# Optimization experiments

Hardware: AMD Instinct MI355X
Metric: run time of the kernel (lower is better)

The kernel has to match this reference:

```python
import jax, jax.numpy as jnp
import numpy as np
import math

B, S, DM, H, DH = 2, 2048, 1024, 16, 64  # batch, seq, d_model, heads, head_dim


def setup_inputs() -> dict:
    key = jax.random.key(0)
    ks = jax.random.split(key, 4)
    scale = 0.02
    return {
        "hidden_states": jax.random.normal(ks[0], (B, S, DM), jnp.float32),
        "Wq": jax.random.normal(ks[1], (DM, DM), jnp.float32) * scale,
        "bq": jnp.zeros((DM,), jnp.float32),
        "Wk": jax.random.normal(ks[2], (DM, DM), jnp.float32) * scale,
        "bk": jnp.zeros((DM,), jnp.float32),
        "Wv": jax.random.normal(ks[3], (DM, DM), jnp.float32) * scale,
        "bv": jnp.zeros((DM,), jnp.float32),
    }


def reference(hidden_states, Wq, bq, Wk, bk, Wv, bv):
    b, s, _ = hidden_states.shape

    def proj(W, bias):
        # torch Linear: x @ W.T + b, then transpose_for_scores -> [B,H,S,Dh]
        x = hidden_states @ W.T + bias
        return x.reshape(b, s, H, DH).transpose(0, 2, 1, 3)

    query = proj(Wq, bq)
    key = proj(Wk, bk)
    value = proj(Wv, bv)

    # qk_matmul input calibration stats (abs-max over whole tensor)
    q_max = jax.lax.stop_gradient(jnp.max(jnp.abs(query)))
    kT_max = jax.lax.stop_gradient(jnp.max(jnp.abs(key)))  # transpose doesn't change abs-max

    attn_weights = jnp.einsum('bhqd,bhkd->bhqk', query, key)  # [B,H,S,S]
    qk_out_max = jax.lax.stop_gradient(jnp.max(jnp.abs(attn_weights)))

    attn_weights = attn_weights / math.sqrt(DH)
    attn_weights = jax.nn.softmax(attn_weights.astype(jnp.float32), axis=-1).astype(query.dtype)
    # eval mode: dropout p=0.0; head_mask is None

    # v_matmul input stats; note source also records attn_weights abs-max as 'v_matmul_out' (faithful)
    aw_max = jax.lax.stop_gradient(jnp.max(jnp.abs(attn_weights)))
    v_max = jax.lax.stop_gradient(jnp.max(jnp.abs(value)))
    v_out_max = aw_max  # source bug: re-reads attn_weights for v_matmul_out

    attn_output = jnp.einsum('bhqk,bhkd->bhqd', attn_weights, value)
    attn_output = attn_output.transpose(0, 2, 1, 3).reshape(b, s, H * DH)
    return attn_output, q_max, kT_max, qk_out_max, aw_max, v_max, v_out_max
```

## Files before the change

### kernel.cpp

```cpp
#include <hip/hip_runtime.h>
#include <hip/hip_bf16.h>
#include <stdint.h>

typedef __attribute__((ext_vector_type(8))) short short8;
typedef __attribute__((ext_vector_type(4))) short short4v;
typedef __attribute__((ext_vector_type(4))) float f32x4;

#define MFMA(a, b, c) __builtin_amdgcn_mfma_f32_16x16x32_bf16((a), (b), (c), 0, 0, 0)

#define C1 0.18033688011112042f
#define INV_C1 5.545177444479562f

static __device__ __forceinline__ unsigned int f2bf2(float x, float y) {
  union { __hip_bfloat162 h; unsigned int u; } c;
  c.h = __float22bfloat162_rn(make_float2(x, y));
  return c.u;
}

static __device__ __forceinline__ void atomic_max_f32(float* addr, float v) {
  atomicMax((int*)addr, __float_as_int(v));
}

static __device__ __forceinline__ void gl_lds16(const void* g, void* l) {
  __builtin_amdgcn_global_load_lds(
      (const __attribute__((address_space(1))) void*)g,
      (__attribute__((address_space(3))) void*)l, 16, 0, 0);
}

__global__ __launch_bounds__(256) void k_cvt(
    const float* __restrict__ X, const float* __restrict__ Wq,
    const float* __restrict__ Wk, const float* __restrict__ Wv,
    short* __restrict__ Xb, short* __restrict__ Wb) {
  const int y = blockIdx.y;
  const float* src;
  short* dst;
  int n;
  if (y == 0) {
    src = X; dst = Xb; n = 4096 * 1024;
  } else {
    src = (y == 1) ? Wq : (y == 2) ? Wk : Wv;
    dst = Wb + (y - 1) * 1048576;
    n = 1048576;
  }
  const int i = (blockIdx.x * 256 + threadIdx.x) * 8;
  if (i >= n) return;
  const float4 a = *(const float4*)(src + i);
  const float4 b = *(const float4*)(src + i + 4);
  union { unsigned int u[4]; short8 s; } P;
  P.u[0] = f2bf2(a.x, a.y);
  P.u[1] = f2bf2(a.z, a.w);
  P.u[2] = f2bf2(b.x, b.y);
  P.u[3] = f2bf2(b.z, b.w);
  *(short8*)(dst + i) = P.s;
}

__global__ __launch_bounds__(256) void k_qkv(
    const short* __restrict__ Xb, const short* __restrict__ Wball,
    const float* __restrict__ bq, const float* __restrict__ bk,
    const float* __restrict__ bv,
    short* __restrict__ Qo, short* __restrict__ Ko, short* __restrict__ Vo,
    float* __restrict__ stats) {
  const int fid = (blockIdx.z * 32 + blockIdx.y) * 8 + blockIdx.x;
  const int sid = (fid & 7) * 96 + (fid >> 3);
  const int colb = sid & 7;
  const int zy = sid >> 3;
  const int z = zy >> 5;
  const int yb = zy & 31;

  const short* W = Wball + z * 1048576;
  const float* bias = (z == 0) ? bq : (z == 1) ? bk : bv;
  short* out = (z == 0) ? Qo : (z == 1) ? Ko : Vo;
  const bool qk = (z < 2);

  __shared__ __align__(16) short AB[8192];
  __shared__ float red[4];

  const int t = threadIdx.x;
  const int lane = t & 63;
  const int w = t >> 6;
  const int l16 = lane & 15, quad = lane >> 4;
  const int wr = (w >> 1) * 64, wc = (w & 1) * 64;
  const int row0 = yb * 128;
  const int col0 = colb * 128;

  const int grow = w * 16 + (lane >> 2);
  const int gcol = (lane & 3) * 8;
  const short* ag = Xb + (size_t)(row0 + grow) * 1024 + gcol;
  const short* bg = W + (size_t)(col0 + grow) * 1024 + gcol;
  short* al = AB + w * 512;
  short* bl = AB + 4096 + w * 512;

  const int f0o = qk ? (4096 + wc * 32) : (wr * 32);
  const int f1o = qk ? (wr * 32) : (4096 + wc * 32);

  f32x4 acc[4][4];
#pragma unroll
  for (int i = 0; i < 4; ++i)
#pragma unroll
    for (int j = 0; j < 4; ++j) acc[i][j] = {0.f, 0.f, 0.f, 0.f};

  for (int kk = 0; kk < 32; ++kk) {
    __syncthreads();
    const int k0 = kk * 32;
#pragma unroll
    for (int c = 0; c < 2; ++c) {
      gl_lds16(ag + c * 65536 + k0, al + c * 2048);
      gl_lds16(bg + c * 65536 + k0, bl + c * 2048);
    }
    __syncthreads();
    short8 fr0[4], fr1[4];
#pragma unroll
    for (int a = 0; a < 4; ++a)
      fr0[a] = *(const short8*)&AB[f0o + (a * 16 + l16) * 32 + quad * 8];
#pragma unroll
    for (int b = 0; b < 4; ++b)
      fr1[b] = *(const short8*)&AB[f1o + (b * 16 + l16) * 32 + quad * 8];
#pragma unroll
    for (int a = 0; a < 4; ++a)
#pragma unroll
      for (int b = 0; b < 4; ++b) acc[a][b] = MFMA(fr0[a], fr1[b], acc[a][b]);
  }

  const float qs = (z == 0) ? C1 : 1.0f;
  float amax = 0.f;
  if (qk) {
#pragma unroll
    for (int a = 0; a < 4; ++a) {
      const int dg = col0 + wc + a * 16 + quad * 4;
      const float4 b4 = *(const float4*)&bias[dg];
      const int h = dg >> 6, dl = dg & 63;
#pragma unroll
      for (int b = 0; b < 4; ++b) {
        const int sg = row0 + wr + b * 16 + l16;
        const float y0 = acc[a][b][0] + b4.x;
        const float y1 = acc[a][b][1] + b4.y;
        const float y2 = acc[a][b][2] + b4.z;
        const float y3 = acc[a][b][3] + b4.w;
        amax = fmaxf(amax, fmaxf(fmaxf(fabsf(y0), fabsf(y1)), fmaxf(fabsf(y2), fabsf(y3))));
        union { unsigned int u[2]; short4v s; } pk;
        pk.u[0] = f2bf2(y0 * qs, y1 * qs);
        pk.u[1] = f2bf2(y2 * qs, y3 * qs);
        const int bidx = sg >> 11, sl = sg & 2047;
        *(short4v*)&out[(size_t)(((bidx << 4) | h) * 2048 + sl) * 64 + dl] = pk.s;
      }
    }
  } else {
#pragma unroll
    for (int a = 0; a < 4; ++a) {
      const int sg = row0 + wr + a * 16 + quad * 4;
      const int bidx = sg >> 11, sl = sg & 2047;
#pragma unroll
      for (int b = 0; b < 4; ++b) {
        const int dg = col0 + wc + b * 16 + l16;
        const float bvf = bias[dg];
        const int h = dg >> 6, dl = dg & 63;
        const float y0 = acc[a][b][0] + bvf;
        const float y1 = acc[a][b][1] + bvf;
        const float y2 = acc[a][b][2] + bvf;
        const float y3 = acc[a][b][3] + bvf;
        amax = fmaxf(amax, fmaxf(fmaxf(fabsf(y0), fabsf(y1)), fmaxf(fabsf(y2), fabsf(y3))));
        union { unsigned int u[2]; short4v s; } pk;
        pk.u[0] = f2bf2(y0, y1);
        pk.u[1] = f2bf2(y2, y3);
        *(short4v*)&out[(size_t)(((bidx << 4) | h) * 64 + dl) * 2048 + sl] = pk.s;
      }
    }
  }
#pragma unroll
  for (int off = 32; off > 0; off >>= 1)
    amax = fmaxf(amax, __shfl_xor(amax, off, 64));
  if (lane == 0) red[w] = amax;
  __syncthreads();
  if (t == 0) {
    float m = fmaxf(fmaxf(red[0], red[1]), fmaxf(red[2], red[3]));
    atomic_max_f32(&stats[z], m);
  }
}

__global__ __launch_bounds__(512) void k_attn(
    const short* __restrict__ Q, const short* __restrict__ K,
    const short* __restrict__ V, float* __restrict__ O,
    float* __restrict__ stats) {
  const int fid = blockIdx.y * 16 + blockIdx.x;
  const int sid = ((fid & 7) << 6) + (fid >> 3);
  const int bh = sid >> 4;
  const int q0 = (sid & 15) << 7;
  const short* Qh = Q + (size_t)bh * 2048 * 64;
  const short* Kh = K + (size_t)bh * 2048 * 64;
  const short* Vh = V + (size_t)bh * 2048 * 64;

  __shared__ __align__(16) short Ks[64 * 72];
  __shared__ __align__(16) short Vts[64 * 72];
  __shared__ __align__(16) short Ps[8][16 * 72];
  __shared__ float redA[8], redB[8];

  const int t = threadIdx.x, lane = t & 63, w = t >> 6;
  const int l16 = lane & 15, quad = lane >> 4;
  const int srow = t >> 3, scol = (t & 7) * 8;
  short* myPs = &Ps[w][0];

  short8 bq0, bq1;
  {
    const short* qsrc = Qh + (q0 + w * 16 + l16) * 64 + quad * 8;
    bq0 = *(const short8*)qsrc;
    bq1 = *(const short8*)(qsrc + 32);
  }

  float m_lane = -1e30f, l_lane = 0.f, xmin_lane = 1e30f;
  f32x4 o_acc[4];
#pragma unroll
  for (int jn = 0; jn < 4; ++jn) o_acc[jn] = {0.f, 0.f, 0.f, 0.f};
  const f32x4 zero = {0.f, 0.f, 0.f, 0.f};

  short8 pk0 = *(const short8*)(Kh + srow * 64 + scol);
  short8 pv0 = *(const short8*)(Vh + srow * 2048 + scol);

  for (int kt = 0; kt < 32; ++kt) {
    __syncthreads();
    *(short8*)&Ks[srow * 72 + scol] = pk0;
    *(short8*)&Vts[srow * 72 + scol] = pv0;
    {
      const int ktn = (kt < 31) ? kt + 1 : 31;
      pk0 = *(const short8*)(Kh + (ktn * 64 + srow) * 64 + scol);
      pv0 = *(const short8*)(Vh + srow * 2048 + ktn * 64 + scol);
    }
    __syncthreads();

    f32x4 sacc[4];
#pragma unroll
    for (int j = 0; j < 4; ++j) {
      short8 kf0 = *(const short8*)&Ks[(j * 16 + l16) * 72 + quad * 8];
      short8 kf1 = *(const short8*)&Ks[(j * 16 + l16) * 72 + 32 + quad * 8];
      sacc[j] = MFMA(kf1, bq1, MFMA(kf0, bq0, zero));
    }

    {
      float pmax = m_lane, psum = l_lane, xmn = xmin_lane;
#pragma unroll
      for (int j = 0; j < 4; ++j) {
        const float x0 = sacc[j][0], x1 = sacc[j][1];
        const float x2 = sacc[j][2], x3 = sacc[j][3];
        pmax = fmaxf(pmax, fmaxf(fmaxf(x0, x1), fmaxf(x2, x3)));
        xmn = fminf(xmn, fminf(fminf(x0, x1), fminf(x2, x3)));
        const float e0 = exp2f(x0), e1 = exp2f(x1);
        const float e2 = exp2f(x2), e3 = exp2f(x3);
        psum += (e0 + e1) + (e2 + e3);
        union { unsigned int u[2]; short4v s; } pk;
        pk.u[0] = f2bf2(e0, e1);
        pk.u[1] = f2bf2(e2, e3);
        *(short4v*)&myPs[l16 * 72 + j * 16 + quad * 4] = pk.s;
      }
      m_lane = pmax;
      l_lane = psum;
      xmin_lane = xmn;
    }
    asm volatile("" ::: "memory");

#pragma unroll
    for (int tstep = 0; tstep < 2; ++tstep) {
      short8 ap = *(const short8*)&myPs[l16 * 72 + tstep * 32 + quad * 8];
#pragma unroll
      for (int jn = 0; jn < 4; ++jn) {
        short8 vf = *(const short8*)&Vts[(jn * 16 + l16) * 72 + tstep * 32 + quad * 8];
        o_acc[jn] = MFMA(ap, vf, o_acc[jn]);
      }
    }
    asm volatile("" ::: "memory");
  }

  float l = l_lane;
  l += __shfl_xor(l, 16, 64);
  l += __shfl_xor(l, 32, 64);
  float m = m_lane;
  m = fmaxf(m, __shfl_xor(m, 16, 64));
  m = fmaxf(m, __shfl_xor(m, 32, 64));
  float xm = xmin_lane;
  xm = fminf(xm, __shfl_xor(xm, 16, 64));
  xm = fminf(xm, __shfl_xor(xm, 32, 64));
  float aw = exp2f(m) / l;
  float qkx = fmaxf(m, -xm);

  const int bidx = bh >> 4, h = bh & 15;
  float linv[4];
#pragma unroll
  for (int r = 0; r < 4; ++r)
    linv[r] = 1.0f / __shfl(l, quad * 4 + r, 16);
#pragma unroll
  for (int jn = 0; jn < 4; ++jn) {
    const int d = jn * 16 + l16;
#pragma unroll
    for (int r = 0; r < 4; ++r) {
      const int s_row = q0 + w * 16 + quad * 4 + r;
      O[((size_t)(bidx * 2048 + s_row) * 1024) + h * 64 + d] =
          o_acc[jn][r] * linv[r];
    }
  }

#pragma unroll
  for (int off = 32; off > 0; off >>= 1) {
    qkx = fmaxf(qkx, __shfl_xor(qkx, off, 64));
    aw = fmaxf(aw, __shfl_xor(aw, off, 64));
  }
  if (lane == 0) {
    redA[w] = qkx;
    redB[w] = aw;
  }
  __syncthreads();
  if (t == 0) {
    float a = redA[0], b = redB[0];
#pragma unroll
    for (int i = 1; i < 8; ++i) {
      a = fmaxf(a, redA[i]);
      b = fmaxf(b, redB[i]);
    }
    atomic_max_f32(&stats[3], a * INV_C1);
    atomic_max_f32(&stats[4], b);
  }
}

__global__ void k_fin(const float* __restrict__ stats, float* __restrict__ out) {
  const int i = threadIdx.x;
  if (i == 0) out[0] = stats[0];
  if (i == 1) out[1] = stats[1];
  if (i == 2) out[2] = stats[3];
  if (i == 3) out[3] = stats[4];
  if (i == 4) out[4] = stats[2];
  if (i == 5) out[5] = stats[4];
}

extern "C" void kernel_launch(void* const* d_in, const int* in_sizes, int n_in,
                              void* d_out, int out_size, void* d_ws, size_t ws_size,
                              hipStream_t stream) {
  const float* X = (const float*)d_in[0];
  const float* Wq = (const float*)d_in[1];
  const float* bq = (const float*)d_in[2];
  const float* Wk = (const float*)d_in[3];
  const float* bk = (const float*)d_in[4];
  const float* Wv = (const float*)d_in[5];
  const float* bv = (const float*)d_in[6];
  float* out = (float*)d_out;

  float* stats = (float*)d_ws;
  short* base = (short*)((char*)d_ws + 4096);
  short* Qb = base;
  short* Kb = base + 4194304;
  short* Vb = base + 8388608;
  short* Xb = base + 12582912;
  short* Wb = base + 16777216;

  k_cvt<<<dim3(2048, 4), 256, 0, stream>>>(X, Wq, Wk, Wv, Xb, Wb);
  k_qkv<<<dim3(8, 32, 3), 256, 0, stream>>>(Xb, Wb, bq, bk, bv, Qb, Kb, Vb, stats);
  k_attn<<<dim3(16, 32), 512, 0, stream>>>(Qb, Kb, Vb, out, stats);
  k_fin<<<1, 64, 0, stream>>>(stats, out + 4194304);
}
```

Before: 208.7 us.

## Shrink attention blocks to 4 waves and load K fragments directly into registers

The attention kernel now runs 256-thread blocks, each covering 64 query rows, so twice as many blocks are launched and occupancy is hinted at 4 blocks per CU. The K tile is no longer staged in shared memory. Each lane loads its MFMA K fragments straight from global memory into registers and prefetches the next tile's fragments after the QK MFMAs. This removes LDS traffic for K and shrinks shared memory, at the cost of more register pressure and every wave loading K separately from global/L2 instead of sharing it.

```diff
diff --git a/kernel.cpp b/kernel.cpp
--- a/kernel.cpp
+++ b/kernel.cpp
@@ -177,26 +177,25 @@
   }
 }
 
-__global__ __launch_bounds__(512) void k_attn(
+__global__ __launch_bounds__(256, 4) void k_attn(
     const short* __restrict__ Q, const short* __restrict__ K,
     const short* __restrict__ V, float* __restrict__ O,
     float* __restrict__ stats) {
-  const int fid = blockIdx.y * 16 + blockIdx.x;
-  const int sid = ((fid & 7) << 6) + (fid >> 3);
-  const int bh = sid >> 4;
-  const int q0 = (sid & 15) << 7;
+  const int fid = blockIdx.y * 32 + blockIdx.x;
+  const int sid = ((fid & 7) << 7) + (fid >> 3);
+  const int bh = sid >> 5;
+  const int q0 = (sid & 31) << 6;
   const short* Qh = Q + (size_t)bh * 2048 * 64;
   const short* Kh = K + (size_t)bh * 2048 * 64;
   const short* Vh = V + (size_t)bh * 2048 * 64;
 
-  __shared__ __align__(16) short Ks[64 * 72];
   __shared__ __align__(16) short Vts[64 * 72];
-  __shared__ __align__(16) short Ps[8][16 * 72];
-  __shared__ float redA[8], redB[8];
+  __shared__ __align__(16) short Ps[4][16 * 72];
+  __shared__ float redA[4], redB[4];
 
   const int t = threadIdx.x, lane = t & 63, w = t >> 6;
   const int l16 = lane & 15, quad = lane >> 4;
-  const int srow = t >> 3, scol = (t & 7) * 8;
+  const int srow = t >> 2, scol = (t & 3) * 16;
   short* myPs = &Ps[w][0];
 
   short8 bq0, bq1;
@@ -206,32 +205,47 @@
     bq1 = *(const short8*)(qsrc + 32);
   }
 
+  const short* kg = Kh + l16 * 64 + quad * 8;
+
   float m_lane = -1e30f, l_lane = 0.f, xmin_lane = 1e30f;
   f32x4 o_acc[4];
 #pragma unroll
   for (int jn = 0; jn < 4; ++jn) o_acc[jn] = {0.f, 0.f, 0.f, 0.f};
   const f32x4 zero = {0.f, 0.f, 0.f, 0.f};
 
-  short8 pk0 = *(const short8*)(Kh + srow * 64 + scol);
   short8 pv0 = *(const short8*)(Vh + srow * 2048 + scol);
+  short8 pv1 = *(const short8*)(Vh + srow * 2048 + scol + 8);
+  short8 kf[4][2];
+#pragma unroll
+  for (int j = 0; j < 4; ++j)
+#pragma unroll
+    for (int hk = 0; hk < 2; ++hk)
+      kf[j][hk] = *(const short8*)(kg + j * 1024 + hk * 32);
 
   for (int kt = 0; kt < 32; ++kt) {
     __syncthreads();
-    *(short8*)&Ks[srow * 72 + scol] = pk0;
     *(short8*)&Vts[srow * 72 + scol] = pv0;
+    *(short8*)&Vts[srow * 72 + scol + 8] = pv1;
+    const int ktn = (kt < 31) ? kt + 1 : 31;
     {
-      const int ktn = (kt < 31) ? kt + 1 : 31;
-      pk0 = *(const short8*)(Kh + (ktn * 64 + srow) * 64 + scol);
-      pv0 = *(const short8*)(Vh + srow * 2048 + ktn * 64 + scol);
+      const short* vsrc = Vh + srow * 2048 + ktn * 64 + scol;
+      pv0 = *(const short8*)vsrc;
+      pv1 = *(const short8*)(vsrc + 8);
     }
     __syncthreads();
 
     f32x4 sacc[4];
 #pragma unroll
-    for (int j = 0; j < 4; ++j) {
-      short8 kf0 = *(const short8*)&Ks[(j * 16 + l16) * 72 + quad * 8];
-      short8 kf1 = *(const short8*)&Ks[(j * 16 + l16) * 72 + 32 + quad * 8];
-      sacc[j] = MFMA(kf1, bq1, MFMA(kf0, bq0, zero));
+    for (int j = 0; j < 4; ++j)
+      sacc[j] = MFMA(kf[j][1], bq1, MFMA(kf[j][0], bq0, zero));
+
+    {
+      const short* kgn = kg + ktn * 4096;
+#pragma unroll
+      for (int j = 0; j < 4; ++j)
+#pragma unroll
+        for (int hk = 0; hk < 2; ++hk)
+          kf[j][hk] = *(const short8*)(kgn + j * 1024 + hk * 32);
     }
 
     {
@@ -240,8 +254,8 @@
       for (int j = 0; j < 4; ++j) {
         const float x0 = sacc[j][0], x1 = sacc[j][1];
         const float x2 = sacc[j][2], x3 = sacc[j][3];
-        pmax = fmaxf(pmax, fmaxf(fmaxf(x0, x1), fmaxf(x2, x3)));
-        xmn = fminf(xmn, fminf(fminf(x0, x1), fminf(x2, x3)));
+        pmax = fmaxf(fmaxf(x0, fmaxf(x1, x2)), fmaxf(x3, pmax));
+        xmn = fminf(fminf(x0, fminf(x1, x2)), fminf(x3, xmn));
         const float e0 = exp2f(x0), e1 = exp2f(x1);
         const float e2 = exp2f(x2), e3 = exp2f(x3);
         psum += (e0 + e1) + (e2 + e3);
@@ -307,12 +321,8 @@
   }
   __syncthreads();
   if (t == 0) {
-    float a = redA[0], b = redB[0];
-#pragma unroll
-    for (int i = 1; i < 8; ++i) {
-      a = fmaxf(a, redA[i]);
-      b = fmaxf(b, redB[i]);
-    }
+    float a = fmaxf(fmaxf(redA[0], redA[1]), fmaxf(redA[2], redA[3]));
+    float b = fmaxf(fmaxf(redB[0], redB[1]), fmaxf(redB[2], redB[3]));
     atomic_max_f32(&stats[3], a * INV_C1);
     atomic_max_f32(&stats[4], b);
   }
@@ -350,6 +360,6 @@
 
   k_cvt<<<dim3(2048, 4), 256, 0, stream>>>(X, Wq, Wk, Wv, Xb, Wb);
   k_qkv<<<dim3(8, 32, 3), 256, 0, stream>>>(Xb, Wb, bq, bk, bv, Qb, Kb, Vb, stats);
-  k_attn<<<dim3(16, 32), 512, 0, stream>>>(Qb, Kb, Vb, out, stats);
+  k_attn<<<dim3(32, 32), 256, 0, stream>>>(Qb, Kb, Vb, out, stats);
   k_fin<<<1, 64, 0, stream>>>(stats, out + 4194304);
 }
```

After: 266.6 us. +27.8%, slower.
